# Optimization experiments

Hardware: AMD Instinct MI355X
Metric: run time of the kernel (lower is better)

## Reference

```python
import jax, jax.numpy as jnp
import numpy as np

N = 50000       # nodes
E = 800000      # edges (before self-loops)
F_IN = 128      # num_features
HID = 32        # hidden_dim per head
HEADS = 8
C = 40          # num_classes
NEG_SLOPE = 0.2 # PyG GATConv default leaky_relu slope


def setup_inputs() -> dict:
    key = jax.random.key(0)
    ks = jax.random.split(key, 10)
    x = jax.random.normal(ks[0], (N, F_IN), jnp.float32)
    edge_index = jax.random.randint(ks[1], (2, E), 0, N, dtype=jnp.int64)
    W1 = jax.random.normal(ks[2], (F_IN, HEADS * HID), jnp.float32) * np.float32(1.0 / np.sqrt(F_IN))
    a1_src = jax.random.normal(ks[3], (HEADS, HID), jnp.float32) * 0.1
    a1_dst = jax.random.normal(ks[4], (HEADS, HID), jnp.float32) * 0.1
    b1 = jnp.zeros((HEADS * HID,), jnp.float32)
    W2 = jax.random.normal(ks[5], (HEADS * HID, C), jnp.float32) * np.float32(1.0 / np.sqrt(HEADS * HID))
    a2_src = jax.random.normal(ks[6], (1, C), jnp.float32) * 0.1
    a2_dst = jax.random.normal(ks[7], (1, C), jnp.float32) * 0.1
    b2 = jnp.zeros((C,), jnp.float32)
    return {"x": x, "edge_index": edge_index,
            "W1": W1, "a1_src": a1_src, "a1_dst": a1_dst, "b1": b1,
            "W2": W2, "a2_src": a2_src, "a2_dst": a2_dst, "b2": b2}


def gat_conv(x, edge_index, W, a_src, a_dst, bias):
    """PyG-style GATConv (concat heads, add_self_loops=True), inference mode (no dropout)."""
    n = x.shape[0]
    heads, out_dim = a_src.shape
    ar = jnp.arange(n, dtype=edge_index.dtype)
    src = jnp.concatenate([edge_index[0], ar])   # [E+N]
    dst = jnp.concatenate([edge_index[1], ar])   # [E+N]
    h = (x @ W).reshape(n, heads, out_dim)       # [N, H, D]
    alpha_src = jnp.einsum('nhd,hd->nh', h, a_src)  # [N, H]
    alpha_dst = jnp.einsum('nhd,hd->nh', h, a_dst)  # [N, H]
    e = jax.nn.leaky_relu(alpha_src[src] + alpha_dst[dst], NEG_SLOPE)  # [E+N, H]
    # segment softmax over edges grouped by destination node
    m = jax.ops.segment_max(e, dst, num_segments=n)          # [N, H]
    ex = jnp.exp(e - m[dst])                                  # [E+N, H]
    s = jax.ops.segment_sum(ex, dst, num_segments=n)          # [N, H]
    alpha = ex / (s[dst] + 1e-16)                              # [E+N, H]
    msg = h[src] * alpha[..., None]                            # [E+N, H, D]
    out = jax.ops.segment_sum(msg, dst, num_segments=n)       # [N, H, D]
    return out.reshape(n, heads * out_dim) + bias


def reference(x, edge_index, W1, a1_src, a1_dst, b1, W2, a2_src, a2_dst, b2):
    h = jax.nn.elu(gat_conv(x, edge_index, W1, a1_src, a1_dst, b1))
    # F.dropout is identity in eval mode
    return gat_conv(h, edge_index, W2, a2_src, a2_dst, b2)
```

## Files before the change

### kernel.cpp

```cpp
#include <hip/hip_runtime.h>
#include <math.h>

#define F_IN 128
#define HID 32
#define HEADS 8
#define HD 256
#define NC 40
#define NCP 48
#define H2S 64
#define NEG 0.2f

typedef _Float16 half8 __attribute__((ext_vector_type(8)));
typedef _Float16 half4v __attribute__((ext_vector_type(4)));
typedef float f32x4 __attribute__((ext_vector_type(4)));

__device__ __forceinline__ float leaky(float v) { return v > 0.0f ? v : NEG * v; }
__device__ __forceinline__ float2 up2(unsigned int u) {
    union { unsigned int u; _Float16 h[2]; } c; c.u = u;
    return make_float2((float)c.h[0], (float)c.h[1]);
}

__global__ __launch_bounds__(256) void prep_count_k(const float* __restrict__ W1,
        const float* __restrict__ W2, _Float16* __restrict__ W1t,
        _Float16* __restrict__ W2t, const int* __restrict__ ei,
        int* __restrict__ deg, int* __restrict__ ord, int E) {
    int i = blockIdx.x * 256 + threadIdx.x;
    if (i < HD * F_IN) {
        int c = i >> 7, k = i & 127;
        W1t[i] = (_Float16)W1[k * HD + c];
    }
    int j = i - HD * F_IN;
    if (j >= 0 && j < NCP * HD) {
        int c = j >> 8, k = j & 255;
        W2t[j] = (c < NC) ? (_Float16)W2[k * NC + c] : (_Float16)0.0f;
    }
    int e = i - (HD * F_IN + NCP * HD);
    if (e >= 0 && e < E) {
        int dst = ei[E + e];
        ord[e] = atomicAdd(&deg[dst], 1);
    }
}

__global__ __launch_bounds__(256) void scan1_k(const int* __restrict__ deg,
        int* __restrict__ rowptr, int* __restrict__ partial, int N) {
    __shared__ int tmp[256];
    int t = threadIdx.x;
    int idx = blockIdx.x * 256 + t;
    int v = (idx < N) ? (deg[idx] + 1) : 0;
    tmp[t] = v;
    __syncthreads();
#pragma unroll
    for (int off = 1; off < 256; off <<= 1) {
        int add = (t >= off) ? tmp[t - off] : 0;
        __syncthreads();
        tmp[t] += add;
        __syncthreads();
    }
    if (idx < N) rowptr[idx] = tmp[t] - v;
    if (t == 255) partial[blockIdx.x] = tmp[255];
}

__global__ __launch_bounds__(256) void scan2_k(int* __restrict__ partial, int P) {
    __shared__ int tmp[256];
    int t = threadIdx.x;
    int v = (t < P) ? partial[t] : 0;
    tmp[t] = v;
    __syncthreads();
#pragma unroll
    for (int off = 1; off < 256; off <<= 1) {
        int add = (t >= off) ? tmp[t - off] : 0;
        __syncthreads();
        tmp[t] += add;
        __syncthreads();
    }
    if (t < P) partial[t] = tmp[t] - v;
}

__global__ __launch_bounds__(256) void scan3_k(int* __restrict__ rowptr,
        const int* __restrict__ partial, int* __restrict__ esrc, int N, int EN) {
    int idx = blockIdx.x * 256 + threadIdx.x;
    if (idx >= N) return;
    int rp = rowptr[idx] + partial[blockIdx.x];
    rowptr[idx] = rp;
    esrc[rp] = idx;
    if (idx == 0) rowptr[N] = EN;
}

__global__ __launch_bounds__(256) void scatter_k(const int* __restrict__ ei,
        const int* __restrict__ rowptr, const int* __restrict__ ord,
        int* __restrict__ esrc, int E) {
    int e = blockIdx.x * 256 + threadIdx.x;
    if (e >= E) return;
    int src = ei[e], dst = ei[E + e];
    esrc[rowptr[dst] + 1 + ord[e]] = src;
}

__global__ __launch_bounds__(256) void gemm1_k(const float* __restrict__ x,
        const _Float16* __restrict__ W1t, _Float16* __restrict__ H1, int N) {
    int t = threadIdx.x;
    int w = t >> 6, l = t & 63;
    int quad = l >> 4, lr = l & 15;
    int rowA = blockIdx.x * 64 + w * 16 + lr;
    int rowL = rowA < N ? rowA : N - 1;

    half8 af[4];
    const float* xr = x + (size_t)rowL * F_IN + quad * 8;
#pragma unroll
    for (int s = 0; s < 4; ++s) {
        float4 u = *(const float4*)(xr + s * 32);
        float4 v = *(const float4*)(xr + s * 32 + 4);
        half8 a;
        a[0] = (_Float16)u.x; a[1] = (_Float16)u.y;
        a[2] = (_Float16)u.z; a[3] = (_Float16)u.w;
        a[4] = (_Float16)v.x; a[5] = (_Float16)v.y;
        a[6] = (_Float16)v.z; a[7] = (_Float16)v.w;
        af[s] = a;
    }

    int rowC0 = blockIdx.x * 64 + w * 16 + quad * 4;
#pragma unroll
    for (int tt = 0; tt < 16; ++tt) {
        f32x4 acc = {0.0f, 0.0f, 0.0f, 0.0f};
        const _Float16* wp = W1t + (size_t)(tt * 16 + lr) * F_IN + quad * 8;
#pragma unroll
        for (int s = 0; s < 4; ++s) {
            half8 b = *(const half8*)(wp + s * 32);
            acc = __builtin_amdgcn_mfma_f32_16x16x32_f16(af[s], b, acc, 0, 0, 0);
        }
#pragma unroll
        for (int r = 0; r < 4; ++r) {
            int rr = rowC0 + r;
            if (rr < N) H1[(size_t)rr * HD + tt * 16 + lr] = (_Float16)acc[r];
        }
    }
}

__global__ __launch_bounds__(256) void alpha1_k(const _Float16* __restrict__ H1,
        const float* __restrict__ a1s, const float* __restrict__ a1d,
        float* __restrict__ asrc, float* __restrict__ adst, int N) {
    int id = blockIdx.x * 256 + threadIdx.x;
    int node = id >> 3, h = id & 7;
    if (node >= N) return;
    const uint4* hp = (const uint4*)(H1 + (size_t)node * HD + h * HID);
    const float* as = a1s + h * HID;
    const float* ad = a1d + h * HID;
    float ps = 0.0f, pd = 0.0f;
#pragma unroll
    for (int q = 0; q < 4; ++q) {
        uint4 u = hp[q];
        float2 f0 = up2(u.x), f1 = up2(u.y), f2 = up2(u.z), f3 = up2(u.w);
        int b = q * 8;
        ps = fmaf(f0.x, as[b + 0], ps); pd = fmaf(f0.x, ad[b + 0], pd);
        ps = fmaf(f0.y, as[b + 1], ps); pd = fmaf(f0.y, ad[b + 1], pd);
        ps = fmaf(f1.x, as[b + 2], ps); pd = fmaf(f1.x, ad[b + 2], pd);
        ps = fmaf(f1.y, as[b + 3], ps); pd = fmaf(f1.y, ad[b + 3], pd);
        ps = fmaf(f2.x, as[b + 4], ps); pd = fmaf(f2.x, ad[b + 4], pd);
        ps = fmaf(f2.y, as[b + 5], ps); pd = fmaf(f2.y, ad[b + 5], pd);
        ps = fmaf(f3.x, as[b + 6], ps); pd = fmaf(f3.x, ad[b + 6], pd);
        ps = fmaf(f3.y, as[b + 7], ps); pd = fmaf(f3.y, ad[b + 7], pd);
    }
    asrc[id] = ps; adst[id] = pd;
}

__global__ __launch_bounds__(256) void agg1_k(const int* __restrict__ esrc,
        const int* __restrict__ rowptr, const float* __restrict__ asrc,
        const float* __restrict__ adst, const _Float16* __restrict__ H1,
        const float* __restrict__ b1, _Float16* __restrict__ out1, int N) {
    int t = threadIdx.x;
    int lane = t & 63;
    int dst = blockIdx.x * 4 + (t >> 6);
    if (dst >= N) return;
    int j = lane & 7;
    int h = lane >> 3;
    int start = rowptr[dst], end = rowptr[dst + 1];
    float adh = adst[dst * HEADS + h];

    float s = 0.0f;
    for (int e = start + j; e < end; e += 8)
        s += __expf(leaky(asrc[esrc[e] * HEADS + h] + adh));
    s += __shfl_xor(s, 1, 64);
    s += __shfl_xor(s, 2, 64);
    s += __shfl_xor(s, 4, 64);
    float inv = 1.0f / (s + 1e-16f);

    float a0 = 0.0f, a1 = 0.0f, a2 = 0.0f, a3 = 0.0f;
    int e = start;
    for (; e + 3 < end; e += 4) {
        int s0 = esrc[e], s1 = esrc[e + 1], s2 = esrc[e + 2], s3 = esrc[e + 3];
        float al0 = asrc[s0 * HEADS + h];
        float al1 = asrc[s1 * HEADS + h];
        float al2 = asrc[s2 * HEADS + h];
        float al3 = asrc[s3 * HEADS + h];
        uint2 h0 = *(const uint2*)(H1 + (size_t)s0 * HD + lane * 4);
        uint2 h1 = *(const uint2*)(H1 + (size_t)s1 * HD + lane * 4);
        uint2 h2 = *(const uint2*)(H1 + (size_t)s2 * HD + lane * 4);
        uint2 h3 = *(const uint2*)(H1 + (size_t)s3 * HD + lane * 4);
        float w0 = __expf(leaky(al0 + adh)) * inv;
        float w1 = __expf(leaky(al1 + adh)) * inv;
        float w2 = __expf(leaky(al2 + adh)) * inv;
        float w3 = __expf(leaky(al3 + adh)) * inv;
        float2 p0 = up2(h0.x), p1 = up2(h0.y);
        a0 = fmaf(p0.x, w0, a0); a1 = fmaf(p0.y, w0, a1);
        a2 = fmaf(p1.x, w0, a2); a3 = fmaf(p1.y, w0, a3);
        p0 = up2(h1.x); p1 = up2(h1.y);
        a0 = fmaf(p0.x, w1, a0); a1 = fmaf(p0.y, w1, a1);
        a2 = fmaf(p1.x, w1, a2); a3 = fmaf(p1.y, w1, a3);
        p0 = up2(h2.x); p1 = up2(h2.y);
        a0 = fmaf(p0.x, w2, a0); a1 = fmaf(p0.y, w2, a1);
        a2 = fmaf(p1.x, w2, a2); a3 = fmaf(p1.y, w2, a3);
        p0 = up2(h3.x); p1 = up2(h3.y);
        a0 = fmaf(p0.x, w3, a0); a1 = fmaf(p0.y, w3, a1);
        a2 = fmaf(p1.x, w3, a2); a3 = fmaf(p1.y, w3, a3);
    }
    for (; e < end; ++e) {
        int s0 = esrc[e];
        float al0 = asrc[s0 * HEADS + h];
        uint2 h0 = *(const uint2*)(H1 + (size_t)s0 * HD + lane * 4);
        float w0 = __expf(leaky(al0 + adh)) * inv;
        float2 p0 = up2(h0.x), p1 = up2(h0.y);
        a0 = fmaf(p0.x, w0, a0); a1 = fmaf(p0.y, w0, a1);
        a2 = fmaf(p1.x, w0, a2); a3 = fmaf(p1.y, w0, a3);
    }
    float4 bv = *(const float4*)(b1 + lane * 4);
    float o0 = a0 + bv.x, o1 = a1 + bv.y, o2 = a2 + bv.z, o3 = a3 + bv.w;
    o0 = o0 > 0.0f ? o0 : expm1f(o0);
    o1 = o1 > 0.0f ? o1 : expm1f(o1);
    o2 = o2 > 0.0f ? o2 : expm1f(o2);
    o3 = o3 > 0.0f ? o3 : expm1f(o3);
    half4v o;
    o[0] = (_Float16)o0; o[1] = (_Float16)o1;
    o[2] = (_Float16)o2; o[3] = (_Float16)o3;
    *(half4v*)(out1 + (size_t)dst * HD + lane * 4) = o;
}

__global__ __launch_bounds__(256) void gemm2_k(const _Float16* __restrict__ out1,
        const _Float16* __restrict__ W2t, const float* __restrict__ a2s,
        const float* __restrict__ a2d, _Float16* __restrict__ H2h,
        float* __restrict__ asrc2, float* __restrict__ adst2, int N) {
    int t = threadIdx.x;
    int w = t >> 6, l = t & 63;
    int quad = l >> 4, lr = l & 15;
    int rowA = blockIdx.x * 64 + w * 16 + lr;
    int rowL = rowA < N ? rowA : N - 1;

    half8 af[8];
    const _Float16* ar = out1 + (size_t)rowL * HD + quad * 8;
#pragma unroll
    for (int s = 0; s < 8; ++s) af[s] = *(const half8*)(ar + s * 32);

    f32x4 acc[3];
#pragma unroll
    for (int tt = 0; tt < 3; ++tt) {
        f32x4 a = {0.0f, 0.0f, 0.0f, 0.0f};
        const _Float16* wp = W2t + (size_t)(tt * 16 + lr) * HD + quad * 8;
#pragma unroll
        for (int s = 0; s < 8; ++s) {
            half8 b = *(const half8*)(wp + s * 32);
            a = __builtin_amdgcn_mfma_f32_16x16x32_f16(af[s], b, a, 0, 0, 0);
        }
        acc[tt] = a;
    }

    float a2sv[3], a2dv[3];
#pragma unroll
    for (int tt = 0; tt < 3; ++tt) {
        int col = tt * 16 + lr;
        a2sv[tt] = (col < NC) ? a2s[col] : 0.0f;
        a2dv[tt] = (col < NC) ? a2d[col] : 0.0f;
    }
    int rowC0 = blockIdx.x * 64 + w * 16 + quad * 4;
#pragma unroll
    for (int r = 0; r < 4; ++r) {
        int row = rowC0 + r;
        if (row >= N) break;
        float ps = 0.0f, pd = 0.0f;
#pragma unroll
        for (int tt = 0; tt < 3; ++tt) {
            int col = tt * 16 + lr;
            float v = acc[tt][r];
            H2h[(size_t)row * H2S + col] = (_Float16)v;
            ps = fmaf(v, a2sv[tt], ps);
            pd = fmaf(v, a2dv[tt], pd);
        }
        ps += __shfl_xor(ps, 1, 64); ps += __shfl_xor(ps, 2, 64);
        ps += __shfl_xor(ps, 4, 64); ps += __shfl_xor(ps, 8, 64);
        pd += __shfl_xor(pd, 1, 64); pd += __shfl_xor(pd, 2, 64);
        pd += __shfl_xor(pd, 4, 64); pd += __shfl_xor(pd, 8, 64);
        if (lr == 0) { asrc2[row] = ps; adst2[row] = pd; }
    }
}

__global__ __launch_bounds__(256) void agg2_k(const int* __restrict__ esrc,
        const int* __restrict__ rowptr, const float* __restrict__ asrc,
        const float* __restrict__ adst, const _Float16* __restrict__ H2h,
        const float* __restrict__ b2, float* __restrict__ dout, int N) {
    int t = threadIdx.x;
    int g = t >> 6, lane = t & 63;
    int dst = blockIdx.x * 4 + g;
    if (dst >= N) return;
    int start = rowptr[dst], end = rowptr[dst + 1];
    float adst_v = adst[dst];

    float sloc = 0.0f;
    for (int e = start + lane; e < end; e += 64)
        sloc += __expf(leaky(asrc[esrc[e]] + adst_v));
#pragma unroll
    for (int off = 32; off > 0; off >>= 1)
        sloc += __shfl_xor(sloc, off, 64);
    float inv = 1.0f / (sloc + 1e-16f);

    float acc = 0.0f;
    int e = start;
    for (; e + 3 < end; e += 4) {
        int s0 = esrc[e], s1 = esrc[e + 1], s2 = esrc[e + 2], s3 = esrc[e + 3];
        float al0 = asrc[s0], al1 = asrc[s1], al2 = asrc[s2], al3 = asrc[s3];
        float v0 = (float)H2h[(size_t)s0 * H2S + lane];
        float v1 = (float)H2h[(size_t)s1 * H2S + lane];
        float v2 = (float)H2h[(size_t)s2 * H2S + lane];
        float v3 = (float)H2h[(size_t)s3 * H2S + lane];
        float w0 = __expf(leaky(al0 + adst_v)) * inv;
        float w1 = __expf(leaky(al1 + adst_v)) * inv;
        float w2 = __expf(leaky(al2 + adst_v)) * inv;
        float w3 = __expf(leaky(al3 + adst_v)) * inv;
        acc = fmaf(v0, w0, acc);
        acc = fmaf(v1, w1, acc);
        acc = fmaf(v2, w2, acc);
        acc = fmaf(v3, w3, acc);
    }
    for (; e < end; ++e) {
        int s0 = esrc[e];
        float w0 = __expf(leaky(asrc[s0] + adst_v)) * inv;
        acc = fmaf((float)H2h[(size_t)s0 * H2S + lane], w0, acc);
    }
    if (lane < NC) dout[(size_t)dst * NC + lane] = acc + b2[lane];
}

extern "C" void kernel_launch(void* const* d_in, const int* in_sizes, int n_in,
                              void* d_out, int out_size, void* d_ws, size_t ws_size,
                              hipStream_t stream) {
    const float* x   = (const float*)d_in[0];
    const int*   ei  = (const int*)d_in[1];
    const float* W1  = (const float*)d_in[2];
    const float* a1s = (const float*)d_in[3];
    const float* a1d = (const float*)d_in[4];
    const float* b1  = (const float*)d_in[5];
    const float* W2  = (const float*)d_in[6];
    const float* a2s = (const float*)d_in[7];
    const float* a2d = (const float*)d_in[8];
    const float* b2  = (const float*)d_in[9];
    float* dout = (float*)d_out;

    int N = in_sizes[0] / F_IN;
    int E = in_sizes[1] / 2;
    int EN = E + N;
    int NB = (N + 255) / 256;

    char* base = (char*)d_ws;
    size_t off = 0;
    auto carve = [&](size_t bytes) { char* p = base + off; off += (bytes + 255) & ~(size_t)255; return p; };
    _Float16* H1   = (_Float16*)carve((size_t)N * HD * 2);
    _Float16* W1t  = (_Float16*)carve((size_t)HD * F_IN * 2);
    _Float16* W2t  = (_Float16*)carve((size_t)NCP * HD * 2);
    _Float16* out1 = (_Float16*)carve((size_t)N * HD * 2);
    _Float16* H2h  = (_Float16*)carve((size_t)N * H2S * 2);
    float* asrc1  = (float*)carve((size_t)N * HEADS * 4);
    float* adst1  = (float*)carve((size_t)N * HEADS * 4);
    float* asrc2  = (float*)carve((size_t)N * 4);
    float* adst2  = (float*)carve((size_t)N * 4);
    int*   deg    = (int*)carve((size_t)N * 4);
    int*   ord    = (int*)carve((size_t)E * 4);
    int*   rowptr = (int*)carve((size_t)(N + 1) * 4);
    int*   part   = (int*)carve((size_t)NB * 4);
    int*   esrc   = (int*)carve((size_t)EN * 4);

    hipMemsetAsync(deg, 0, (size_t)N * 4, stream);
    int prep_total = HD * F_IN + NCP * HD + E;
    hipLaunchKernelGGL(prep_count_k, dim3((prep_total + 255) / 256), dim3(256), 0, stream,
                       W1, W2, W1t, W2t, ei, deg, ord, E);
    hipLaunchKernelGGL(scan1_k, dim3(NB), dim3(256), 0, stream, deg, rowptr, part, N);
    hipLaunchKernelGGL(scan2_k, dim3(1), dim3(256), 0, stream, part, NB);
    hipLaunchKernelGGL(scan3_k, dim3(NB), dim3(256), 0, stream, rowptr, part, esrc, N, EN);
    hipLaunchKernelGGL(scatter_k, dim3((E + 255) / 256), dim3(256), 0, stream, ei, rowptr, ord, esrc, E);

    hipLaunchKernelGGL(gemm1_k, dim3((N + 63) / 64), dim3(256), 0, stream,
                       x, W1t, H1, N);
    hipLaunchKernelGGL(alpha1_k, dim3((N * HEADS + 255) / 256), dim3(256), 0, stream,
                       H1, a1s, a1d, asrc1, adst1, N);
    hipLaunchKernelGGL(agg1_k, dim3((N + 3) / 4), dim3(256), 0, stream,
                       esrc, rowptr, asrc1, adst1, H1, b1, out1, N);

    hipLaunchKernelGGL(gemm2_k, dim3((N + 63) / 64), dim3(256), 0, stream,
                       out1, W2t, a2s, a2d, H2h, asrc2, adst2, N);
    hipLaunchKernelGGL(agg2_k, dim3((N + 3) / 4), dim3(256), 0, stream,
                       esrc, rowptr, asrc2, adst2, H2h, b2, dout, N);
}
```

Baseline: 327.9 us.

## Fold attention projections into GEMM1, merge scans, deepen agg1 unroll

Precomputes W1·a_src/a_dst as an extra 16-column projection matrix so gemm1 produces the attention logits directly with one more MFMA tile, removing the separate alpha1 kernel and its reread of H1. Replaces the three-kernel scan with one 1024-thread single-block scan to cut launches. Also unrolls the agg1 edge loop by 8 to issue more independent gathers. The single-block scan serializes about 49 elements per thread, and computing the logits from the unrounded product instead of fp16 H1 changes rounding slightly.

```diff
diff --git a/kernel.cpp b/kernel.cpp
--- a/kernel.cpp
+++ b/kernel.cpp
@@ -21,9 +21,11 @@
 }
 
 __global__ __launch_bounds__(256) void prep_count_k(const float* __restrict__ W1,
-        const float* __restrict__ W2, _Float16* __restrict__ W1t,
-        _Float16* __restrict__ W2t, const int* __restrict__ ei,
-        int* __restrict__ deg, int* __restrict__ ord, int E) {
+        const float* __restrict__ W2, const float* __restrict__ a1s,
+        const float* __restrict__ a1d, _Float16* __restrict__ W1t,
+        _Float16* __restrict__ W2t, _Float16* __restrict__ Pt,
+        const int* __restrict__ ei, int* __restrict__ deg,
+        int* __restrict__ ord, int E) {
     int i = blockIdx.x * 256 + threadIdx.x;
     if (i < HD * F_IN) {
         int c = i >> 7, k = i & 127;
@@ -39,51 +41,48 @@
         int dst = ei[E + e];
         ord[e] = atomicAdd(&deg[dst], 1);
     }
-}
-
-__global__ __launch_bounds__(256) void scan1_k(const int* __restrict__ deg,
-        int* __restrict__ rowptr, int* __restrict__ partial, int N) {
-    __shared__ int tmp[256];
-    int t = threadIdx.x;
-    int idx = blockIdx.x * 256 + t;
-    int v = (idx < N) ? (deg[idx] + 1) : 0;
-    tmp[t] = v;
+    int p = i - (HD * F_IN + NCP * HD + E);
+    if (p >= 0 && p < 16 * F_IN) {
+        int pj = p >> 7, k = p & 127;
+        int h = pj & 7;
+        const float* av = (pj < 8) ? (a1s + h * HID) : (a1d + h * HID);
+        const float* wr = W1 + (size_t)k * HD + h * HID;
+        float acc = 0.0f;
+#pragma unroll 8
+        for (int d = 0; d < HID; ++d) acc = fmaf(wr[d], av[d], acc);
+        Pt[pj * F_IN + k] = (_Float16)acc;
+    }
+}
+
+__global__ __launch_bounds__(1024) void scan_k(const int* __restrict__ deg,
+        int* __restrict__ rowptr, int* __restrict__ esrc, int N, int EN) {
+    __shared__ int ssum[1024];
+    int t = threadIdx.x;
+    int per = (N + 1023) / 1024;
+    int b0 = t * per;
+    int loc = 0;
+    for (int i = 0; i < per; ++i) {
+        int idx = b0 + i;
+        if (idx < N) loc += deg[idx] + 1;
+    }
+    ssum[t] = loc;
     __syncthreads();
-#pragma unroll
-    for (int off = 1; off < 256; off <<= 1) {
-        int add = (t >= off) ? tmp[t - off] : 0;
+    for (int off = 1; off < 1024; off <<= 1) {
+        int add = (t >= off) ? ssum[t - off] : 0;
         __syncthreads();
-        tmp[t] += add;
+        ssum[t] += add;
         __syncthreads();
     }
-    if (idx < N) rowptr[idx] = tmp[t] - v;
-    if (t == 255) partial[blockIdx.x] = tmp[255];
-}
-
-__global__ __launch_bounds__(256) void scan2_k(int* __restrict__ partial, int P) {
-    __shared__ int tmp[256];
-    int t = threadIdx.x;
-    int v = (t < P) ? partial[t] : 0;
-    tmp[t] = v;
-    __syncthreads();
-#pragma unroll
-    for (int off = 1; off < 256; off <<= 1) {
-        int add = (t >= off) ? tmp[t - off] : 0;
-        __syncthreads();
-        tmp[t] += add;
-        __syncthreads();
-    }
-    if (t < P) partial[t] = tmp[t] - v;
-}
-
-__global__ __launch_bounds__(256) void scan3_k(int* __restrict__ rowptr,
-        const int* __restrict__ partial, int* __restrict__ esrc, int N, int EN) {
-    int idx = blockIdx.x * 256 + threadIdx.x;
-    if (idx >= N) return;
-    int rp = rowptr[idx] + partial[blockIdx.x];
-    rowptr[idx] = rp;
-    esrc[rp] = idx;
-    if (idx == 0) rowptr[N] = EN;
+    int run = ssum[t] - loc;
+    for (int i = 0; i < per; ++i) {
+        int idx = b0 + i;
+        if (idx < N) {
+            rowptr[idx] = run;
+            esrc[run] = idx;
+            run += deg[idx] + 1;
+        }
+    }
+    if (t == 0) rowptr[N] = EN;
 }
 
 __global__ __launch_bounds__(256) void scatter_k(const int* __restrict__ ei,
@@ -96,7 +95,9 @@
 }
 
 __global__ __launch_bounds__(256) void gemm1_k(const float* __restrict__ x,
-        const _Float16* __restrict__ W1t, _Float16* __restrict__ H1, int N) {
+        const _Float16* __restrict__ W1t, const _Float16* __restrict__ Pt,
+        _Float16* __restrict__ H1, float* __restrict__ asrc,
+        float* __restrict__ adst, int N) {
     int t = threadIdx.x;
     int w = t >> 6, l = t & 63;
     int quad = l >> 4, lr = l & 15;
@@ -133,33 +134,23 @@
             if (rr < N) H1[(size_t)rr * HD + tt * 16 + lr] = (_Float16)acc[r];
         }
     }
-}
-
-__global__ __launch_bounds__(256) void alpha1_k(const _Float16* __restrict__ H1,
-        const float* __restrict__ a1s, const float* __restrict__ a1d,
-        float* __restrict__ asrc, float* __restrict__ adst, int N) {
-    int id = blockIdx.x * 256 + threadIdx.x;
-    int node = id >> 3, h = id & 7;
-    if (node >= N) return;
-    const uint4* hp = (const uint4*)(H1 + (size_t)node * HD + h * HID);
-    const float* as = a1s + h * HID;
-    const float* ad = a1d + h * HID;
-    float ps = 0.0f, pd = 0.0f;
-#pragma unroll
-    for (int q = 0; q < 4; ++q) {
-        uint4 u = hp[q];
-        float2 f0 = up2(u.x), f1 = up2(u.y), f2 = up2(u.z), f3 = up2(u.w);
-        int b = q * 8;
-        ps = fmaf(f0.x, as[b + 0], ps); pd = fmaf(f0.x, ad[b + 0], pd);
-        ps = fmaf(f0.y, as[b + 1], ps); pd = fmaf(f0.y, ad[b + 1], pd);
-        ps = fmaf(f1.x, as[b + 2], ps); pd = fmaf(f1.x, ad[b + 2], pd);
-        ps = fmaf(f1.y, as[b + 3], ps); pd = fmaf(f1.y, ad[b + 3], pd);
-        ps = fmaf(f2.x, as[b + 4], ps); pd = fmaf(f2.x, ad[b + 4], pd);
-        ps = fmaf(f2.y, as[b + 5], ps); pd = fmaf(f2.y, ad[b + 5], pd);
-        ps = fmaf(f3.x, as[b + 6], ps); pd = fmaf(f3.x, ad[b + 6], pd);
-        ps = fmaf(f3.y, as[b + 7], ps); pd = fmaf(f3.y, ad[b + 7], pd);
-    }
-    asrc[id] = ps; adst[id] = pd;
+    {
+        f32x4 acc = {0.0f, 0.0f, 0.0f, 0.0f};
+        const _Float16* pp = Pt + (size_t)lr * F_IN + quad * 8;
+#pragma unroll
+        for (int s = 0; s < 4; ++s) {
+            half8 b = *(const half8*)(pp + s * 32);
+            acc = __builtin_amdgcn_mfma_f32_16x16x32_f16(af[s], b, acc, 0, 0, 0);
+        }
+#pragma unroll
+        for (int r = 0; r < 4; ++r) {
+            int rr = rowC0 + r;
+            if (rr < N) {
+                if (lr < 8) asrc[rr * HEADS + lr] = acc[r];
+                else        adst[rr * HEADS + (lr - 8)] = acc[r];
+            }
+        }
+    }
 }
 
 __global__ __launch_bounds__(256) void agg1_k(const int* __restrict__ esrc,
@@ -185,32 +176,39 @@
 
     float a0 = 0.0f, a1 = 0.0f, a2 = 0.0f, a3 = 0.0f;
     int e = start;
+    for (; e + 7 < end; e += 8) {
+        int si[8]; float al[8]; uint2 hv[8];
+#pragma unroll
+        for (int q = 0; q < 8; ++q) si[q] = esrc[e + q];
+#pragma unroll
+        for (int q = 0; q < 8; ++q) {
+            al[q] = asrc[si[q] * HEADS + h];
+            hv[q] = *(const uint2*)(H1 + (size_t)si[q] * HD + lane * 4);
+        }
+#pragma unroll
+        for (int q = 0; q < 8; ++q) {
+            float w = __expf(leaky(al[q] + adh)) * inv;
+            float2 p0 = up2(hv[q].x), p1 = up2(hv[q].y);
+            a0 = fmaf(p0.x, w, a0); a1 = fmaf(p0.y, w, a1);
+            a2 = fmaf(p1.x, w, a2); a3 = fmaf(p1.y, w, a3);
+        }
+    }
     for (; e + 3 < end; e += 4) {
-        int s0 = esrc[e], s1 = esrc[e + 1], s2 = esrc[e + 2], s3 = esrc[e + 3];
-        float al0 = asrc[s0 * HEADS + h];
-        float al1 = asrc[s1 * HEADS + h];
-        float al2 = asrc[s2 * HEADS + h];
-        float al3 = asrc[s3 * HEADS + h];
-        uint2 h0 = *(const uint2*)(H1 + (size_t)s0 * HD + lane * 4);
-        uint2 h1 = *(const uint2*)(H1 + (size_t)s1 * HD + lane * 4);
-        uint2 h2 = *(const uint2*)(H1 + (size_t)s2 * HD + lane * 4);
-        uint2 h3 = *(const uint2*)(H1 + (size_t)s3 * HD + lane * 4);
-        float w0 = __expf(leaky(al0 + adh)) * inv;
-        float w1 = __expf(leaky(al1 + adh)) * inv;
-        float w2 = __expf(leaky(al2 + adh)) * inv;
-        float w3 = __expf(leaky(al3 + adh)) * inv;
-        float2 p0 = up2(h0.x), p1 = up2(h0.y);
-        a0 = fmaf(p0.x, w0, a0); a1 = fmaf(p0.y, w0, a1);
-        a2 = fmaf(p1.x, w0, a2); a3 = fmaf(p1.y, w0, a3);
-        p0 = up2(h1.x); p1 = up2(h1.y);
-        a0 = fmaf(p0.x, w1, a0); a1 = fmaf(p0.y, w1, a1);
-        a2 = fmaf(p1.x, w1, a2); a3 = fmaf(p1.y, w1, a3);
-        p0 = up2(h2.x); p1 = up2(h2.y);
-        a0 = fmaf(p0.x, w2, a0); a1 = fmaf(p0.y, w2, a1);
-        a2 = fmaf(p1.x, w2, a2); a3 = fmaf(p1.y, w2, a3);
-        p0 = up2(h3.x); p1 = up2(h3.y);
-        a0 = fmaf(p0.x, w3, a0); a1 = fmaf(p0.y, w3, a1);
-        a2 = fmaf(p1.x, w3, a2); a3 = fmaf(p1.y, w3, a3);
+        int si[4]; float al[4]; uint2 hv[4];
+#pragma unroll
+        for (int q = 0; q < 4; ++q) si[q] = esrc[e + q];
+#pragma unroll
+        for (int q = 0; q < 4; ++q) {
+            al[q] = asrc[si[q] * HEADS + h];
+            hv[q] = *(const uint2*)(H1 + (size_t)si[q] * HD + lane * 4);
+        }
+#pragma unroll
+        for (int q = 0; q < 4; ++q) {
+            float w = __expf(leaky(al[q] + adh)) * inv;
+            float2 p0 = up2(hv[q].x), p1 = up2(hv[q].y);
+            a0 = fmaf(p0.x, w, a0); a1 = fmaf(p0.y, w, a1);
+            a2 = fmaf(p1.x, w, a2); a3 = fmaf(p1.y, w, a3);
+        }
     }
     for (; e < end; ++e) {
         int s0 = esrc[e];
@@ -353,7 +351,6 @@
     int N = in_sizes[0] / F_IN;
     int E = in_sizes[1] / 2;
     int EN = E + N;
-    int NB = (N + 255) / 256;
 
     char* base = (char*)d_ws;
     size_t off = 0;
@@ -361,6 +358,7 @@
     _Float16* H1   = (_Float16*)carve((size_t)N * HD * 2);
     _Float16* W1t  = (_Float16*)carve((size_t)HD * F_IN * 2);
     _Float16* W2t  = (_Float16*)carve((size_t)NCP * HD * 2);
+    _Float16* Pt   = (_Float16*)carve((size_t)16 * F_IN * 2);
     _Float16* out1 = (_Float16*)carve((size_t)N * HD * 2);
     _Float16* H2h  = (_Float16*)carve((size_t)N * H2S * 2);
     float* asrc1  = (float*)carve((size_t)N * HEADS * 4);
@@ -370,22 +368,17 @@
     int*   deg    = (int*)carve((size_t)N * 4);
     int*   ord    = (int*)carve((size_t)E * 4);
     int*   rowptr = (int*)carve((size_t)(N + 1) * 4);
-    int*   part   = (int*)carve((size_t)NB * 4);
     int*   esrc   = (int*)carve((size_t)EN * 4);
 
     hipMemsetAsync(deg, 0, (size_t)N * 4, stream);
-    int prep_total = HD * F_IN + NCP * HD + E;
+    int prep_total = HD * F_IN + NCP * HD + E + 16 * F_IN;
     hipLaunchKernelGGL(prep_count_k, dim3((prep_total + 255) / 256), dim3(256), 0, stream,
-                       W1, W2, W1t, W2t, ei, deg, ord, E);
-    hipLaunchKernelGGL(scan1_k, dim3(NB), dim3(256), 0, stream, deg, rowptr, part, N);
-    hipLaunchKernelGGL(scan2_k, dim3(1), dim3(256), 0, stream, part, NB);
-    hipLaunchKernelGGL(scan3_k, dim3(NB), dim3(256), 0, stream, rowptr, part, esrc, N, EN);
+                       W1, W2, a1s, a1d, W1t, W2t, Pt, ei, deg, ord, E);
+    hipLaunchKernelGGL(scan_k, dim3(1), dim3(1024), 0, stream, deg, rowptr, esrc, N, EN);
     hipLaunchKernelGGL(scatter_k, dim3((E + 255) / 256), dim3(256), 0, stream, ei, rowptr, ord, esrc, E);
 
     hipLaunchKernelGGL(gemm1_k, dim3((N + 63) / 64), dim3(256), 0, stream,
-                       x, W1t, H1, N);
-    hipLaunchKernelGGL(alpha1_k, dim3((N * HEADS + 255) / 256), dim3(256), 0, stream,
-                       H1, a1s, a1d, asrc1, adst1, N);
+                       x, W1t, Pt, H1, asrc1, adst1, N);
     hipLaunchKernelGGL(agg1_k, dim3((N + 3) / 4), dim3(256), 0, stream,
                        esrc, rowptr, asrc1, adst1, H1, b1, out1, N);
 
```

Result: slower. 428.6 us (+30.7%).
